# Performance work log

Hardware: AMD Instinct MI355X
Metric: run time of the kernel (lower is better)

Reference implementation:

```python
import jax, jax.numpy as jnp
import numpy as np

B, D, H, E, TOPK = 65536, 1024, 512, 8, 2
LN_EPS = 1e-5
LB_WEIGHT = 0.01


def setup_inputs() -> dict:
    key = jax.random.key(0)
    ks = jax.random.split(key, 5)
    x = jax.random.normal(ks[0], (B, D), dtype=jnp.float32)
    W1 = jax.random.normal(ks[1], (D, H), dtype=jnp.float32) * 0.02
    b1 = jnp.zeros((H,), dtype=jnp.float32)
    ln_w = jnp.ones((H,), dtype=jnp.float32)
    ln_b = jnp.zeros((H,), dtype=jnp.float32)
    W2 = jax.random.normal(ks[2], (H, E), dtype=jnp.float32) * 0.02
    b2 = jnp.zeros((E,), dtype=jnp.float32)
    return {"x": x, "W1": W1, "b1": b1, "ln_w": ln_w, "ln_b": ln_b, "W2": W2, "b2": b2}


def _gate_logits(x, W1, b1, ln_w, ln_b, W2, b2):
    h = x @ W1 + b1                     # [B, H]
    mu = jnp.mean(h, axis=-1, keepdims=True)
    var = jnp.mean(jnp.square(h - mu), axis=-1, keepdims=True)
    h = (h - mu) * jax.lax.rsqrt(var + LN_EPS) * ln_w + ln_b
    h = jax.nn.gelu(h, approximate=False)  # torch nn.GELU default = exact erf
    return h @ W2 + b2                  # [B, E]


def reference(x, W1, b1, ln_w, ln_b, W2, b2):
    logits = _gate_logits(x, W1, b1, ln_w, ln_b, W2, b2)
    # sparse top-K routing (eval mode: no exploration noise)
    vals, idx = jax.lax.top_k(logits, TOPK)           # [B, K]
    rows = jnp.arange(logits.shape[0])[:, None]
    sparse = jnp.full_like(logits, -jnp.inf).at[rows, idx].set(vals)
    weights = jax.nn.softmax(sparse, axis=-1)         # zeros off top-k
    # Switch-style load-balance loss
    f = (weights > 0).astype(weights.dtype).mean(axis=0)  # fraction routed per expert
    P = weights.mean(axis=0)                              # mean gate prob per expert
    lb_loss = LB_WEIGHT * (E * jnp.sum(f * P))
    return weights, lb_loss
```

## Files before the change

kernel.cpp:

```cpp
#include <hip/hip_runtime.h>
#include <cstdint>
#include <cstddef>


typedef _Float16 f16;
typedef _Float16 f16x4 __attribute__((ext_vector_type(4)));
typedef _Float16 f16x8 __attribute__((ext_vector_type(8)));
typedef float f32x4 __attribute__((ext_vector_type(4)));

#define B_ROWS 65536
#define D_DIM 1024
#define H_DIM 512
#define E_DIM 8
#define BM 64
#define BK 32
#define NCHUNK 32
#define THREADS 512
#define LDP 40
#define IMG_CH (H_DIM * BK)
#define IMG_TOTAL (NCHUNK * IMG_CH)
#define GACC_OFF ((size_t)2 * IMG_TOTAL * sizeof(f16))

__global__ void prep_split(const float* __restrict__ W1,
                           f16* __restrict__ wh, f16* __restrict__ wl) {
  int id = blockIdx.x * 256 + threadIdx.x;
  int h = id & (H_DIM - 1);
  int kg = id >> 9;
  int c = kg >> 2;
  int kk0 = (kg & 3) * 8;
  int k0 = kg * 8;
  f16x8 hv, lv;
#pragma unroll
  for (int j = 0; j < 8; ++j) {
    float v = W1[(size_t)(k0 + j) * H_DIM + h] * 64.0f;
    f16 hi = (f16)v;
    hv[j] = hi;
    lv[j] = (f16)((v - (float)hi) * 256.0f);
  }
  size_t o = (size_t)c * IMG_CH + (size_t)h * BK + kk0;
  *(f16x8*)&wh[o] = hv;
  *(f16x8*)&wl[o] = lv;
}

__global__ void zero_acc(float* __restrict__ acc) {
  if (threadIdx.x < 16) acc[threadIdx.x] = 0.0f;
}

__global__ __launch_bounds__(THREADS, 4) void fused_main(
    const float* __restrict__ x,
    const f16* __restrict__ wh, const f16* __restrict__ wl,
    const float* __restrict__ b1, const float* __restrict__ lnw,
    const float* __restrict__ lnb, const float* __restrict__ W2,
    const float* __restrict__ b2, float* __restrict__ out,
    float* __restrict__ gacc) {
  __shared__ __align__(16) char pool[43584];
  f16* sX = (f16*)pool;

  const int tid = threadIdx.x;
  const int lane = tid & 63;
  const int wv = tid >> 6;
  const int l15 = lane & 15;
  const int l4 = lane >> 4;
  const int64_t row0 = (int64_t)blockIdx.x * BM;

  const int srow = tid >> 3;
  const int sc4 = (tid & 7) * 4;
  const float* xp = x + (row0 + srow) * D_DIM + sc4;
  const int swo = srow * LDP + sc4;

  const int col0 = wv * 64 + l15;
  const f16* whp = wh + (size_t)col0 * BK + l4 * 8;
  const f16* wlp = wl + (size_t)col0 * BK + l4 * 8;

  f32x4 acc[4][4];
#pragma unroll
  for (int m = 0; m < 4; ++m)
#pragma unroll
    for (int n = 0; n < 4; ++n) acc[m][n] = (f32x4){0.f, 0.f, 0.f, 0.f};

  float4 xv = *(const float4*)xp;

  for (int c = 0; c < NCHUNK; ++c) {
    const int bo = (c & 1) * 5120;
    {
      float vv[4] = {xv.x, xv.y, xv.z, xv.w};
      f16x4 hv, lv;
#pragma unroll
      for (int j = 0; j < 4; ++j) {
        float v = vv[j] * 64.0f;
        f16 hh = (f16)v;
        hv[j] = hh;
        lv[j] = (f16)(v - (float)hh);
      }
      *(f16x4*)&sX[bo + swo] = hv;
      *(f16x4*)&sX[bo + 2560 + swo] = lv;
    }
    if (c + 1 < NCHUNK) xv = *(const float4*)(xp + (c + 1) * BK);
    __syncthreads();

    const f16* whc = whp + (size_t)c * IMG_CH;
    const f16* wlc = wlp + (size_t)c * IMG_CH;
    f16x8 bfrag[4];
#pragma unroll
    for (int n = 0; n < 4; ++n) bfrag[n] = *(const f16x8*)(whc + n * 512);
#pragma unroll
    for (int m = 0; m < 4; ++m) {
      const int ao = bo + (m * 16 + l15) * LDP + l4 * 8;
      f16x8 ah = *(const f16x8*)&sX[ao];
      f16x8 al = *(const f16x8*)&sX[ao + 2560];
#pragma unroll
      for (int n = 0; n < 4; ++n) {
        acc[m][n] = __builtin_amdgcn_mfma_f32_16x16x32_f16(ah, bfrag[n], acc[m][n], 0, 0, 0);
        acc[m][n] = __builtin_amdgcn_mfma_f32_16x16x32_f16(al, bfrag[n], acc[m][n], 0, 0, 0);
      }
    }
#pragma unroll
    for (int n = 0; n < 4; ++n) bfrag[n] = *(const f16x8*)(wlc + n * 512);
#pragma unroll
    for (int m = 0; m < 4; ++m) {
      const int ao = bo + (m * 16 + l15) * LDP + l4 * 8;
      f16x8 ah = *(const f16x8*)&sX[ao];
      f16x8 ahs;
#pragma unroll
      for (int j = 0; j < 8; ++j) ahs[j] = ah[j] * (f16)0.00390625f;
#pragma unroll
      for (int n = 0; n < 4; ++n)
        acc[m][n] = __builtin_amdgcn_mfma_f32_16x16x32_f16(ahs, bfrag[n], acc[m][n], 0, 0, 0);
    }
  }
  __syncthreads();

  float* eW2T = (float*)pool;
  float* eB1 = (float*)(pool + 16384);
  float* eLnw = (float*)(pool + 18432);
  float* eLnb = (float*)(pool + 20480);
  float* eStat = (float*)(pool + 22528);
  float* eLog = (float*)(pool + 26624);
  float* eMu = (float*)(pool + 43008);
  float* eRs = (float*)(pool + 43264);
  float* eFP = (float*)(pool + 43520);

  for (int i = tid; i < H_DIM * E_DIM; i += THREADS) {
    int cc = i >> 3, e = i & 7;
    eW2T[e * H_DIM + cc] = W2[i];
  }
  eB1[tid] = b1[tid] * 4096.0f;
  eLnw[tid] = lnw[tid];
  eLnb[tid] = lnb[tid];
  if (tid < 16) eFP[tid] = 0.0f;
  __syncthreads();

#pragma unroll
  for (int n = 0; n < 4; ++n) {
    float bb = eB1[wv * 64 + n * 16 + l15];
#pragma unroll
    for (int m = 0; m < 4; ++m)
#pragma unroll
      for (int r = 0; r < 4; ++r) acc[m][n][r] += bb;
  }

#pragma unroll
  for (int m = 0; m < 4; ++m) {
    float s1[4] = {0, 0, 0, 0};
    float s2[4] = {0, 0, 0, 0};
#pragma unroll
    for (int n = 0; n < 4; ++n)
#pragma unroll
      for (int r = 0; r < 4; ++r) {
        float v = acc[m][n][r];
        s1[r] += v;
        s2[r] = fmaf(v, v, s2[r]);
      }
#pragma unroll
    for (int d = 1; d < 16; d <<= 1)
#pragma unroll
      for (int r = 0; r < 4; ++r) {
        s1[r] += __shfl_xor(s1[r], d);
        s2[r] += __shfl_xor(s2[r], d);
      }
    if (l15 == 0) {
      int rb = m * 16 + l4 * 4;
#pragma unroll
      for (int r = 0; r < 4; ++r) {
        eStat[(wv * 64 + rb + r) * 2 + 0] = s1[r];
        eStat[(wv * 64 + rb + r) * 2 + 1] = s2[r];
      }
    }
  }
  __syncthreads();
  if (tid < BM) {
    float s1 = 0.0f, s2 = 0.0f;
#pragma unroll
    for (int w = 0; w < 8; ++w) {
      s1 += eStat[(w * 64 + tid) * 2 + 0];
      s2 += eStat[(w * 64 + tid) * 2 + 1];
    }
    float mu = s1 * (1.0f / 512.0f);
    float var = s2 * (1.0f / 512.0f) - mu * mu;
    eMu[tid] = mu;
    eRs[tid] = 1.0f / sqrtf(var + (1e-5f * 4096.0f * 4096.0f));
  }
  __syncthreads();

#pragma unroll
  for (int m = 0; m < 4; ++m) {
    float lg[4][8];
#pragma unroll
    for (int r = 0; r < 4; ++r)
#pragma unroll
      for (int e = 0; e < 8; ++e) lg[r][e] = 0.0f;
    int rb = m * 16 + l4 * 4;
    float mu_r[4], rs_r[4];
#pragma unroll
    for (int r = 0; r < 4; ++r) {
      mu_r[r] = eMu[rb + r];
      rs_r[r] = eRs[rb + r];
    }
#pragma unroll
    for (int n = 0; n < 4; ++n) {
      int col = wv * 64 + n * 16 + l15;
      float lw = eLnw[col], lb = eLnb[col];
#pragma unroll
      for (int r = 0; r < 4; ++r) {
        float hn = (acc[m][n][r] - mu_r[r]) * rs_r[r];
        float y = fmaf(hn, lw, lb);
        float g = 0.5f * y * (1.0f + erff(y * 0.70710678118654752440f));
#pragma unroll
        for (int e = 0; e < 8; ++e) lg[r][e] = fmaf(g, eW2T[e * H_DIM + col], lg[r][e]);
      }
    }
#pragma unroll
    for (int d = 1; d < 16; d <<= 1)
#pragma unroll
      for (int r = 0; r < 4; ++r)
#pragma unroll
        for (int e = 0; e < 8; ++e) lg[r][e] += __shfl_xor(lg[r][e], d);
    if (l15 == 0) {
#pragma unroll
      for (int r = 0; r < 4; ++r)
#pragma unroll
        for (int e = 0; e < 8; ++e) eLog[(wv * 64 + rb + r) * 8 + e] = lg[r][e];
    }
  }
  __syncthreads();

  if (tid < BM) {
    float v[8];
#pragma unroll
    for (int e = 0; e < 8; ++e) {
      float s = b2[e];
#pragma unroll
      for (int w = 0; w < 8; ++w) s += eLog[(w * 64 + tid) * 8 + e];
      v[e] = s;
    }
    float m1 = v[0];
    int i1 = 0;
#pragma unroll
    for (int e = 1; e < 8; ++e)
      if (v[e] > m1) { m1 = v[e]; i1 = e; }
    float m2 = -3.0e38f;
    int i2 = -1;
#pragma unroll
    for (int e = 0; e < 8; ++e)
      if (e != i1 && v[e] > m2) { m2 = v[e]; i2 = e; }
    float dd = expf(m2 - m1);
    float inv = 1.0f / (1.0f + dd);
    float wA = inv, wB = dd * inv;
    float o[8];
#pragma unroll
    for (int e = 0; e < 8; ++e)
      o[e] = (e == i1) ? wA : ((e == i2) ? wB : 0.0f);
    float4* op = (float4*)&out[(row0 + tid) * 8];
    op[0] = (float4){o[0], o[1], o[2], o[3]};
    op[1] = (float4){o[4], o[5], o[6], o[7]};
    atomicAdd(&eFP[i1], 1.0f);
    atomicAdd(&eFP[i2], 1.0f);
    atomicAdd(&eFP[8 + i1], wA);
    atomicAdd(&eFP[8 + i2], wB);
  }
  __syncthreads();
  if (tid < 16) atomicAdd(&gacc[tid], eFP[tid]);
}

__global__ void lb_final(const float* __restrict__ gacc, float* __restrict__ out) {
  if (threadIdx.x == 0) {
    const float invB = 1.0f / 65536.0f;
    float s = 0.0f;
#pragma unroll
    for (int e = 0; e < 8; ++e) s += (gacc[e] * invB) * (gacc[8 + e] * invB);
    out[(size_t)B_ROWS * E_DIM] = 0.01f * 8.0f * s;
  }
}

extern "C" void kernel_launch(void* const* d_in, const int* in_sizes, int n_in,
                              void* d_out, int out_size, void* d_ws, size_t ws_size,
                              hipStream_t stream) {
  (void)in_sizes; (void)n_in; (void)out_size; (void)ws_size;
  const float* x = (const float*)d_in[0];
  const float* W1 = (const float*)d_in[1];
  const float* b1 = (const float*)d_in[2];
  const float* lnw = (const float*)d_in[3];
  const float* lnb = (const float*)d_in[4];
  const float* W2 = (const float*)d_in[5];
  const float* b2 = (const float*)d_in[6];
  float* out = (float*)d_out;
  f16* wh = (f16*)d_ws;
  f16* wl = wh + IMG_TOTAL;
  float* gacc = (float*)((char*)d_ws + GACC_OFF);

  zero_acc<<<1, 64, 0, stream>>>(gacc);
  prep_split<<<(D_DIM * H_DIM / 8) / 256, 256, 0, stream>>>(W1, wh, wl);
  fused_main<<<B_ROWS / BM, THREADS, 0, stream>>>(x, wh, wl, b1, lnw, lnb, W2, b2,
                                                  out, gacc);
  lb_final<<<1, 64, 0, stream>>>(gacc, out);
}
```

Measured before the change: 263.7 us.

## Stage 256-wide K super-chunks with 16 waves splitting M and N

Measured after the change: 368.0 us. 39.6% more time.

```diff
diff --git a/kernel.cpp b/kernel.cpp
--- a/kernel.cpp
+++ b/kernel.cpp
@@ -14,11 +14,13 @@
 #define E_DIM 8
 #define BM 64
 #define BK 32
-#define NCHUNK 32
-#define THREADS 512
-#define LDP 40
+#define THREADS 1024
+#define NSUPER 4
+#define KSUP 256
+#define NCH 8
+#define LDSS 260
 #define IMG_CH (H_DIM * BK)
-#define IMG_TOTAL (NCHUNK * IMG_CH)
+#define IMG_TOTAL (32 * IMG_CH)
 #define GACC_OFF ((size_t)2 * IMG_TOTAL * sizeof(f16))
 
 __global__ void prep_split(const float* __restrict__ W1,
@@ -53,123 +55,127 @@
     const float* __restrict__ lnb, const float* __restrict__ W2,
     const float* __restrict__ b2, float* __restrict__ out,
     float* __restrict__ gacc) {
-  __shared__ __align__(16) char pool[43584];
-  f16* sX = (f16*)pool;
+  __shared__ __align__(16) char pool[66560];
+  f16* sXh = (f16*)pool;
+  f16* sXl = (f16*)(pool + 33280);
 
   const int tid = threadIdx.x;
   const int lane = tid & 63;
   const int wv = tid >> 6;
+  const int ng = wv & 7;
+  const int mg = wv >> 3;
   const int l15 = lane & 15;
   const int l4 = lane >> 4;
   const int64_t row0 = (int64_t)blockIdx.x * BM;
 
-  const int srow = tid >> 3;
-  const int sc4 = (tid & 7) * 4;
-  const float* xp = x + (row0 + srow) * D_DIM + sc4;
-  const int swo = srow * LDP + sc4;
-
-  const int col0 = wv * 64 + l15;
-  const f16* whp = wh + (size_t)col0 * BK + l4 * 8;
-  const f16* wlp = wl + (size_t)col0 * BK + l4 * 8;
-
-  f32x4 acc[4][4];
-#pragma unroll
-  for (int m = 0; m < 4; ++m)
+  const int srow = tid >> 4;
+  const int sk0 = (tid & 15) * 16;
+  const int swo = srow * LDSS + sk0;
+
+  const size_t boff = (size_t)(ng * 64 + l15) * BK + l4 * 8;
+
+  f32x4 acc[2][4];
+#pragma unroll
+  for (int m = 0; m < 2; ++m)
 #pragma unroll
     for (int n = 0; n < 4; ++n) acc[m][n] = (f32x4){0.f, 0.f, 0.f, 0.f};
 
-  float4 xv = *(const float4*)xp;
-
-  for (int c = 0; c < NCHUNK; ++c) {
-    const int bo = (c & 1) * 5120;
+  for (int sc = 0; sc < NSUPER; ++sc) {
+    float4 v[4];
     {
-      float vv[4] = {xv.x, xv.y, xv.z, xv.w};
+      const float* xs = x + (row0 + srow) * D_DIM + sc * KSUP + sk0;
+#pragma unroll
+      for (int j = 0; j < 4; ++j) v[j] = *(const float4*)(xs + 4 * j);
+    }
+    __syncthreads();
+#pragma unroll
+    for (int j = 0; j < 4; ++j) {
+      float vv[4] = {v[j].x, v[j].y, v[j].z, v[j].w};
       f16x4 hv, lv;
 #pragma unroll
-      for (int j = 0; j < 4; ++j) {
-        float v = vv[j] * 64.0f;
-        f16 hh = (f16)v;
-        hv[j] = hh;
-        lv[j] = (f16)(v - (float)hh);
-      }
-      *(f16x4*)&sX[bo + swo] = hv;
-      *(f16x4*)&sX[bo + 2560 + swo] = lv;
-    }
-    if (c + 1 < NCHUNK) xv = *(const float4*)(xp + (c + 1) * BK);
+      for (int q = 0; q < 4; ++q) {
+        float t = vv[q] * 64.0f;
+        f16 hh = (f16)t;
+        hv[q] = hh;
+        lv[q] = (f16)(t - (float)hh);
+      }
+      *(f16x4*)&sXh[swo + 4 * j] = hv;
+      *(f16x4*)&sXl[swo + 4 * j] = lv;
+    }
     __syncthreads();
-
-    const f16* whc = whp + (size_t)c * IMG_CH;
-    const f16* wlc = wlp + (size_t)c * IMG_CH;
-    f16x8 bfrag[4];
-#pragma unroll
-    for (int n = 0; n < 4; ++n) bfrag[n] = *(const f16x8*)(whc + n * 512);
-#pragma unroll
-    for (int m = 0; m < 4; ++m) {
-      const int ao = bo + (m * 16 + l15) * LDP + l4 * 8;
-      f16x8 ah = *(const f16x8*)&sX[ao];
-      f16x8 al = *(const f16x8*)&sX[ao + 2560];
+#pragma unroll
+    for (int cc = 0; cc < NCH; ++cc) {
+      const int kg = sc * NCH + cc;
+      const f16* whc = wh + (size_t)kg * IMG_CH + boff;
+      const f16* wlc = wl + (size_t)kg * IMG_CH + boff;
+      f16x8 bh[4], bl[4];
 #pragma unroll
       for (int n = 0; n < 4; ++n) {
-        acc[m][n] = __builtin_amdgcn_mfma_f32_16x16x32_f16(ah, bfrag[n], acc[m][n], 0, 0, 0);
-        acc[m][n] = __builtin_amdgcn_mfma_f32_16x16x32_f16(al, bfrag[n], acc[m][n], 0, 0, 0);
-      }
-    }
-#pragma unroll
-    for (int n = 0; n < 4; ++n) bfrag[n] = *(const f16x8*)(wlc + n * 512);
-#pragma unroll
-    for (int m = 0; m < 4; ++m) {
-      const int ao = bo + (m * 16 + l15) * LDP + l4 * 8;
-      f16x8 ah = *(const f16x8*)&sX[ao];
-      f16x8 ahs;
-#pragma unroll
-      for (int j = 0; j < 8; ++j) ahs[j] = ah[j] * (f16)0.00390625f;
-#pragma unroll
-      for (int n = 0; n < 4; ++n)
-        acc[m][n] = __builtin_amdgcn_mfma_f32_16x16x32_f16(ahs, bfrag[n], acc[m][n], 0, 0, 0);
-    }
-  }
-  __syncthreads();
-
-  float* eW2T = (float*)pool;
-  float* eB1 = (float*)(pool + 16384);
-  float* eLnw = (float*)(pool + 18432);
-  float* eLnb = (float*)(pool + 20480);
-  float* eStat = (float*)(pool + 22528);
-  float* eLog = (float*)(pool + 26624);
-  float* eMu = (float*)(pool + 43008);
-  float* eRs = (float*)(pool + 43264);
-  float* eFP = (float*)(pool + 43520);
-
-  for (int i = tid; i < H_DIM * E_DIM; i += THREADS) {
-    int cc = i >> 3, e = i & 7;
-    eW2T[e * H_DIM + cc] = W2[i];
-  }
-  eB1[tid] = b1[tid] * 4096.0f;
-  eLnw[tid] = lnw[tid];
-  eLnb[tid] = lnb[tid];
+        bh[n] = *(const f16x8*)(whc + n * 512);
+        bl[n] = *(const f16x8*)(wlc + n * 512);
+      }
+#pragma unroll
+      for (int m = 0; m < 2; ++m) {
+        const int o = (mg * 32 + m * 16 + l15) * LDSS + cc * BK + l4 * 8;
+        f16x4 h0 = *(const f16x4*)&sXh[o];
+        f16x4 h1 = *(const f16x4*)&sXh[o + 4];
+        f16x4 l0 = *(const f16x4*)&sXl[o];
+        f16x4 l1 = *(const f16x4*)&sXl[o + 4];
+        f16x8 ah, al, ahs;
+#pragma unroll
+        for (int q = 0; q < 4; ++q) {
+          ah[q] = h0[q]; ah[q + 4] = h1[q];
+          al[q] = l0[q]; al[q + 4] = l1[q];
+        }
+#pragma unroll
+        for (int q = 0; q < 8; ++q) ahs[q] = ah[q] * (f16)0.00390625f;
+#pragma unroll
+        for (int n = 0; n < 4; ++n) {
+          acc[m][n] = __builtin_amdgcn_mfma_f32_16x16x32_f16(ah, bh[n], acc[m][n], 0, 0, 0);
+          acc[m][n] = __builtin_amdgcn_mfma_f32_16x16x32_f16(al, bh[n], acc[m][n], 0, 0, 0);
+          acc[m][n] = __builtin_amdgcn_mfma_f32_16x16x32_f16(ahs, bl[n], acc[m][n], 0, 0, 0);
+        }
+      }
+    }
+  }
+  __syncthreads();
+
+  float* eStat = (float*)pool;
+  float* eLog = (float*)(pool + 4096);
+  float* eMu = (float*)(pool + 20480);
+  float* eRs = (float*)(pool + 20736);
+  float* eFP = (float*)(pool + 20992);
+
+  float bb[4], lw[4], lb[4], w2c[4][8];
+#pragma unroll
+  for (int n = 0; n < 4; ++n) {
+    int col = ng * 64 + n * 16 + l15;
+    bb[n] = b1[col] * 4096.0f;
+    lw[n] = lnw[col];
+    lb[n] = lnb[col];
+    *(float4*)&w2c[n][0] = *(const float4*)&W2[col * 8];
+    *(float4*)&w2c[n][4] = *(const float4*)&W2[col * 8 + 4];
+  }
   if (tid < 16) eFP[tid] = 0.0f;
-  __syncthreads();
-
-#pragma unroll
-  for (int n = 0; n < 4; ++n) {
-    float bb = eB1[wv * 64 + n * 16 + l15];
-#pragma unroll
-    for (int m = 0; m < 4; ++m)
-#pragma unroll
-      for (int r = 0; r < 4; ++r) acc[m][n][r] += bb;
-  }
-
-#pragma unroll
-  for (int m = 0; m < 4; ++m) {
+
+#pragma unroll
+  for (int m = 0; m < 2; ++m)
+#pragma unroll
+    for (int n = 0; n < 4; ++n)
+#pragma unroll
+      for (int r = 0; r < 4; ++r) acc[m][n][r] += bb[n];
+
+#pragma unroll
+  for (int m = 0; m < 2; ++m) {
     float s1[4] = {0, 0, 0, 0};
     float s2[4] = {0, 0, 0, 0};
 #pragma unroll
     for (int n = 0; n < 4; ++n)
 #pragma unroll
       for (int r = 0; r < 4; ++r) {
-        float v = acc[m][n][r];
-        s1[r] += v;
-        s2[r] = fmaf(v, v, s2[r]);
+        float vv = acc[m][n][r];
+        s1[r] += vv;
+        s2[r] = fmaf(vv, vv, s2[r]);
       }
 #pragma unroll
     for (int d = 1; d < 16; d <<= 1)
@@ -179,11 +185,11 @@
         s2[r] += __shfl_xor(s2[r], d);
       }
     if (l15 == 0) {
-      int rb = m * 16 + l4 * 4;
+      int rb = mg * 32 + m * 16 + l4 * 4;
 #pragma unroll
       for (int r = 0; r < 4; ++r) {
-        eStat[(wv * 64 + rb + r) * 2 + 0] = s1[r];
-        eStat[(wv * 64 + rb + r) * 2 + 1] = s2[r];
+        eStat[(ng * 64 + rb + r) * 2 + 0] = s1[r];
+        eStat[(ng * 64 + rb + r) * 2 + 1] = s2[r];
       }
     }
   }
@@ -203,13 +209,13 @@
   __syncthreads();
 
 #pragma unroll
-  for (int m = 0; m < 4; ++m) {
+  for (int m = 0; m < 2; ++m) {
     float lg[4][8];
 #pragma unroll
     for (int r = 0; r < 4; ++r)
 #pragma unroll
       for (int e = 0; e < 8; ++e) lg[r][e] = 0.0f;
-    int rb = m * 16 + l4 * 4;
+    int rb = mg * 32 + m * 16 + l4 * 4;
     float mu_r[4], rs_r[4];
 #pragma unroll
     for (int r = 0; r < 4; ++r) {
@@ -218,15 +224,13 @@
     }
 #pragma unroll
     for (int n = 0; n < 4; ++n) {
-      int col = wv * 64 + n * 16 + l15;
-      float lw = eLnw[col], lb = eLnb[col];
 #pragma unroll
       for (int r = 0; r < 4; ++r) {
         float hn = (acc[m][n][r] - mu_r[r]) * rs_r[r];
-        float y = fmaf(hn, lw, lb);
+        float y = fmaf(hn, lw[n], lb[n]);
         float g = 0.5f * y * (1.0f + erff(y * 0.70710678118654752440f));
 #pragma unroll
-        for (int e = 0; e < 8; ++e) lg[r][e] = fmaf(g, eW2T[e * H_DIM + col], lg[r][e]);
+        for (int e = 0; e < 8; ++e) lg[r][e] = fmaf(g, w2c[n][e], lg[r][e]);
       }
     }
 #pragma unroll
@@ -239,7 +243,7 @@
 #pragma unroll
       for (int r = 0; r < 4; ++r)
 #pragma unroll
-        for (int e = 0; e < 8; ++e) eLog[(wv * 64 + rb + r) * 8 + e] = lg[r][e];
+        for (int e = 0; e < 8; ++e) eLog[(ng * 64 + rb + r) * 8 + e] = lg[r][e];
     }
   }
   __syncthreads();
```
